# Kernel optimization log

Measured on AMD Instinct MI355X. Metric: run time of the kernel, lower is better.

## Reference

```python
import jax, jax.numpy as jnp
import numpy as np

DIM = 1024
NUM_HEADS = 16
NUM_KV_HEADS = 4
HEAD_DIM = DIM // NUM_HEADS
KV_DIM = NUM_KV_HEADS * HEAD_DIM
PARTIAL_ROPE_DIM = 32
ROPE_BASE = 10000.0
LORA_RANK = 4
NUM_LORA_STEPS = 2
LORA_SCALE = 1.0
B, S = 2, 2048


def _rms_norm(x):
    eps = jnp.asarray(jnp.finfo(x.dtype).eps, x.dtype)
    return x * jax.lax.rsqrt(jnp.mean(x * x, axis=-1, keepdims=True) + eps)


def _rope_cos_sin(seq_len, dtype):
    half = PARTIAL_ROPE_DIM // 2
    inv_freq = 1.0 / (ROPE_BASE ** (jnp.arange(0, PARTIAL_ROPE_DIM, 2, dtype=jnp.float32) / PARTIAL_ROPE_DIM))
    t = jnp.arange(seq_len, dtype=jnp.float32)
    freqs = jnp.outer(t, inv_freq)  # [S, half]
    return jnp.cos(freqs).astype(dtype), jnp.sin(freqs).astype(dtype)


def _apply_rope_partial(x, cos, sin):
    # x: [B, H, S, D]; rotate first PARTIAL_ROPE_DIM dims, pass the rest.
    half = PARTIAL_ROPE_DIM // 2
    x1 = x[..., :half]
    x2 = x[..., half:PARTIAL_ROPE_DIM]
    xp = x[..., PARTIAL_ROPE_DIM:]
    c = cos[None, None, :, :]
    s = sin[None, None, :, :]
    return jnp.concatenate([x1 * c + x2 * s, -x1 * s + x2 * c, xp], axis=-1)


def setup_inputs() -> dict:
    key = jax.random.key(0)
    ks = jax.random.split(key, 12)
    std = 0.02
    return {
        "x": jax.random.normal(ks[0], (B, S, DIM), jnp.float32),
        "Wq": jax.random.normal(ks[1], (DIM, DIM), jnp.float32) * std,
        "Wk": jax.random.normal(ks[2], (KV_DIM, DIM), jnp.float32) * std,
        "Wv": jax.random.normal(ks[3], (KV_DIM, DIM), jnp.float32) * std,
        "Wproj": jax.random.normal(ks[4], (DIM, DIM), jnp.float32) * std,
        "q_gain": jnp.full((NUM_HEADS,), 1.0, jnp.float32),
        "lora_A_q": jax.random.normal(ks[5], (NUM_LORA_STEPS, LORA_RANK, DIM), jnp.float32) * std,
        "lora_B_q": jax.random.normal(ks[6], (NUM_LORA_STEPS, DIM, LORA_RANK), jnp.float32) * std,
        "lora_A_v": jax.random.normal(ks[7], (NUM_LORA_STEPS, LORA_RANK, DIM), jnp.float32) * std,
        "lora_B_v": jax.random.normal(ks[8], (NUM_LORA_STEPS, KV_DIM, LORA_RANK), jnp.float32) * std,
        "step_idx": 0,
    }


def reference(x, Wq, Wk, Wv, Wproj, q_gain, lora_A_q, lora_B_q, lora_A_v, lora_B_v, step_idx):
    bsz, seqlen, dim = x.shape
    q = x @ Wq.T
    v = x @ Wv.T
    if 0 <= step_idx < NUM_LORA_STEPS:
        q = q + LORA_SCALE * ((x @ lora_A_q[step_idx].T) @ lora_B_q[step_idx].T)
        v = v + LORA_SCALE * ((x @ lora_A_v[step_idx].T) @ lora_B_v[step_idx].T)
    k = x @ Wk.T

    q = q.reshape(bsz, seqlen, NUM_HEADS, HEAD_DIM).transpose(0, 2, 1, 3)      # [B,H,S,D]
    k = k.reshape(bsz, seqlen, NUM_KV_HEADS, HEAD_DIM).transpose(0, 2, 1, 3)   # [B,Hkv,S,D]
    v = v.reshape(bsz, seqlen, NUM_KV_HEADS, HEAD_DIM).transpose(0, 2, 1, 3)

    q = _rms_norm(q)
    k = _rms_norm(k)

    cos, sin = _rope_cos_sin(seqlen, q.dtype)
    q = _apply_rope_partial(q, cos, sin)
    k = _apply_rope_partial(k, cos, sin)

    q = q * q_gain.astype(q.dtype)[None, :, None, None]

    # GQA causal SDPA
    groups = NUM_HEADS // NUM_KV_HEADS
    qg = q.reshape(bsz, NUM_KV_HEADS, groups, seqlen, HEAD_DIM)
    scale = 1.0 / np.sqrt(HEAD_DIM)
    scores = jnp.einsum('bkgsd,bktd->bkgst', qg, k) * scale  # [B,Hkv,G,S,S]
    causal = jnp.tril(jnp.ones((seqlen, seqlen), bool))
    scores = jnp.where(causal[None, None, None], scores, jnp.asarray(-jnp.inf, scores.dtype))
    attn = jax.nn.softmax(scores, axis=-1)
    y = jnp.einsum('bkgst,bktd->bkgsd', attn, v)
    y = y.reshape(bsz, NUM_HEADS, seqlen, HEAD_DIM).transpose(0, 2, 1, 3).reshape(bsz, seqlen, dim)
    return y @ Wproj.T
```

## Files before the change

kernel.cpp:

```cpp
#include <hip/hip_runtime.h>
#include <hip/hip_bf16.h>
#include <stdint.h>

#define DIM 1024
#define NH 16
#define NKV 4
#define HD 64
#define SEQ 2048
#define BATCH 2
#define RANK 4
#define NSTEPS 2

#define XN      4194304
#define WQ_END  5242880
#define WK_END  5505024
#define WV_END  5767168
#define CVT_BLOCKS 6656
#define LORA_BLOCKS 1024

typedef unsigned short u16;
typedef unsigned int u32;
typedef __attribute__((ext_vector_type(8))) __bf16 bf16x8;
typedef __attribute__((ext_vector_type(4))) float f32x4;

__device__ __forceinline__ float bf2f(u16 v) {
    u32 u = ((u32)v) << 16;
    return __builtin_bit_cast(float, u);
}
__device__ __forceinline__ u16 f2bf(float f) {
    u32 u = __builtin_bit_cast(u32, f);
    u32 r = (u + 0x7fffu + ((u >> 16) & 1u)) >> 16;
    return (u16)r;
}
__device__ __forceinline__ u32 pk2(float a, float b) {
    return (u32)f2bf(a) | ((u32)f2bf(b) << 16);
}
__device__ __forceinline__ u32 pk2t(float a, float b) {
    return __builtin_amdgcn_perm(__builtin_bit_cast(u32, b),
                                 __builtin_bit_cast(u32, a), 0x07060302u);
}
__device__ __forceinline__ void glds16(const u16* g, u16* l) {
    __builtin_amdgcn_global_load_lds(
        (const __attribute__((address_space(1))) u32*)g,
        (__attribute__((address_space(3))) u32*)l, 16, 0, 0);
}

__global__ __launch_bounds__(256) void k_prep(
    const float* __restrict__ x, const float* __restrict__ Wq,
    const float* __restrict__ Wk, const float* __restrict__ Wv,
    const float* __restrict__ Wp, u16* __restrict__ dst,
    const float* __restrict__ Aq, const float* __restrict__ Av,
    const int* __restrict__ step_p, float* __restrict__ tq, float* __restrict__ tv)
{
    int bx = blockIdx.x;
    if (bx < CVT_BLOCKS) {
        int e = (bx * 256 + threadIdx.x) * 4;
        const float* src;
        if (e < XN)          src = x  + e;
        else if (e < WQ_END) src = Wq + (e - XN);
        else if (e < WK_END) src = Wk + (e - WQ_END);
        else if (e < WV_END) src = Wv + (e - WK_END);
        else                 src = Wp + (e - WV_END);
        float4 v = *(const float4*)src;
        *(uint2*)(dst + e) = make_uint2(pk2(v.x, v.y), pk2(v.z, v.w));
        return;
    }
    int wave = ((bx - CVT_BLOCKS) * 256 + threadIdx.x) >> 6;
    int lane = threadIdx.x & 63;
    int step = step_p[0];
    int valid = (step >= 0 && step < NSTEPS);
    int sc = valid ? step : 0;
    const float* xr = x + wave * DIM + lane * 16;
    float xf[16];
#pragma unroll
    for (int q = 0; q < 4; q++) {
        float4 v4 = *(const float4*)(xr + q * 4);
        xf[q * 4 + 0] = v4.x; xf[q * 4 + 1] = v4.y;
        xf[q * 4 + 2] = v4.z; xf[q * 4 + 3] = v4.w;
    }
    float sums[8];
#pragma unroll
    for (int j = 0; j < 8; j++) {
        const float* ar = (j < 4 ? Aq + sc * RANK * DIM + j * DIM
                                 : Av + sc * RANK * DIM + (j - 4) * DIM) + lane * 16;
        float s = 0.f;
#pragma unroll
        for (int q = 0; q < 4; q++) {
            float4 a4 = *(const float4*)(ar + q * 4);
            s += xf[q * 4 + 0] * a4.x + xf[q * 4 + 1] * a4.y
               + xf[q * 4 + 2] * a4.z + xf[q * 4 + 3] * a4.w;
        }
#pragma unroll
        for (int o = 32; o > 0; o >>= 1) s += __shfl_xor(s, o, 64);
        sums[j] = s;
    }
    if (!valid) {
#pragma unroll
        for (int j = 0; j < 8; j++) sums[j] = 0.f;
    }
    if (lane == 0) {
        tq[wave * 4 + 0] = sums[0]; tq[wave * 4 + 1] = sums[1];
        tq[wave * 4 + 2] = sums[2]; tq[wave * 4 + 3] = sums[3];
        tv[wave * 4 + 0] = sums[4]; tv[wave * 4 + 1] = sums[5];
        tv[wave * 4 + 2] = sums[6]; tv[wave * 4 + 3] = sums[7];
    }
}

__global__ __launch_bounds__(256) void k_gemm_qkv(
    const u16* __restrict__ A, const u16* __restrict__ B,
    u16* __restrict__ qkv, u16* __restrict__ vtb,
    const float* __restrict__ tq, const float* __restrict__ Bq,
    const float* __restrict__ tv, const float* __restrict__ Bv,
    const float* __restrict__ gain, const int* __restrict__ step_p)
{
    __shared__ __align__(16) u16 As[16384];
    __shared__ __align__(16) u16 Bs[16384];
    int bx = blockIdx.x;
    int xcd = bx & 7, o = bx >> 3;
    int bm = xcd * 4 + (o & 3);
    int bn = o >> 2;
    int t = threadIdx.x, lane = t & 63, w = t >> 6;
    int wy = w >> 1, wx = w & 1;
    int wb = t & ~63;
    int quad = lane >> 4, n16 = lane & 15;
    f32x4 acc[4][4];
#pragma unroll
    for (int i = 0; i < 4; i++)
#pragma unroll
        for (int j = 0; j < 4; j++) acc[i][j] = (f32x4){0.f, 0.f, 0.f, 0.f};

    int goff[4];
#pragma unroll
    for (int u = 0; u < 4; u++) {
        int idx = u * 256 + t;
        int grp = idx >> 6;
        int q_ = (idx >> 4) & 3, m = idx & 15;
        goff[u] = ((grp >> 1) * 16 + m) * DIM + (grp & 1) * 32 + q_ * 8;
    }
    const u16* Ab = A + bm * 128 * DIM;
    const u16* Bb = B + bn * 128 * DIM;

#pragma unroll 1
    for (int kb = 0; kb < 8; kb++) {
        int k0 = kb * 128;
        __syncthreads();
#pragma unroll
        for (int u = 0; u < 4; u++)
            glds16(Ab + goff[u] + k0, As + (u * 256 + wb) * 8);
#pragma unroll
        for (int u = 0; u < 4; u++)
            glds16(Ab + goff[u] + k0 + 64, As + 8192 + (u * 256 + wb) * 8);
#pragma unroll
        for (int u = 0; u < 4; u++)
            glds16(Bb + goff[u] + k0, Bs + (u * 256 + wb) * 8);
#pragma unroll
        for (int u = 0; u < 4; u++)
            glds16(Bb + goff[u] + k0 + 64, Bs + 8192 + (u * 256 + wb) * 8);
        __syncthreads();
#pragma unroll
        for (int c = 0; c < 4; c++) {
            int sl = (c >> 1) * 8192, ch = c & 1;
            bf16x8 af[4], bfr[4];
#pragma unroll
            for (int i = 0; i < 4; i++)
                af[i] = *(const bf16x8*)(As + sl + (((wy * 4 + i) * 2 + ch) * 64 + lane) * 8);
#pragma unroll
            for (int j = 0; j < 4; j++)
                bfr[j] = *(const bf16x8*)(Bs + sl + (((wx * 4 + j) * 2 + ch) * 64 + lane) * 8);
#pragma unroll
            for (int i = 0; i < 4; i++)
#pragma unroll
                for (int j = 0; j < 4; j++)
                    acc[i][j] = __builtin_amdgcn_mfma_f32_16x16x32_bf16(af[i], bfr[j], acc[i][j], 0, 0, 0);
        }
    }

    int step = step_p[0];
    int sc = (step >= 0 && step < NSTEPS) ? step : 0;
    int row_base = bm * 128 + wy * 64 + quad * 4;

    if (bn < 10) {
        bool isq = (bn < 8);
        int h2 = isq ? (bn * 2 + wx) : ((bn - 8) * 2 + wx);
        int colbase = isq ? (h2 * 64) : (1024 + h2 * 64);
        if (isq) {
            float4 B4[4];
#pragma unroll
            for (int j = 0; j < 4; j++)
                B4[j] = *(const float4*)(Bq + (sc * DIM + h2 * 64 + j * 16 + n16) * RANK);
#pragma unroll
            for (int i = 0; i < 4; i++)
#pragma unroll
                for (int r = 0; r < 4; r++) {
                    float4 t4 = *(const float4*)(tq + (row_base + i * 16 + r) * 4);
#pragma unroll
                    for (int j = 0; j < 4; j++)
                        acc[i][j][r] += t4.x * B4[j].x + t4.y * B4[j].y
                                      + t4.z * B4[j].z + t4.w * B4[j].w;
                }
        }
        float postmul = isq ? (gain[h2] * 0.125f * 1.4426950408889634f) : 1.f;
        float invf = exp2f(-(float)n16 * 0.8304820237218405f);
#pragma unroll
        for (int i = 0; i < 4; i++)
#pragma unroll
            for (int r = 0; r < 4; r++) {
                float s = acc[i][0][r] * acc[i][0][r] + acc[i][1][r] * acc[i][1][r]
                        + acc[i][2][r] * acc[i][2][r] + acc[i][3][r] * acc[i][3][r];
#pragma unroll
                for (int o2 = 1; o2 < 16; o2 <<= 1) s += __shfl_xor(s, o2, 64);
                float rr = rsqrtf(s * (1.f / 64.f) + 1.1920928955078125e-7f);
                int row = row_base + i * 16 + r;
                float v0 = acc[i][0][r] * rr, v1 = acc[i][1][r] * rr;
                float v2 = acc[i][2][r] * rr, v3 = acc[i][3][r] * rr;
                float ang = (float)(row & 2047) * invf;
                float cs = cosf(ang), sn = sinf(ang);
                float o0 = v0 * cs + v1 * sn;
                float o1 = -v0 * sn + v1 * cs;
                u16* dst = qkv + row * 1536 + colbase + n16;
                dst[0]  = f2bf(o0 * postmul);
                dst[16] = f2bf(o1 * postmul);
                dst[32] = f2bf(v2 * postmul);
                dst[48] = f2bf(v3 * postmul);
            }
    } else {
        int g = (bn - 10) * 2 + wx;
        float4 B4[4];
#pragma unroll
        for (int j = 0; j < 4; j++)
            B4[j] = *(const float4*)(Bv + (sc * (NKV * HD) + g * 64 + j * 16 + n16) * RANK);
#pragma unroll
        for (int i = 0; i < 4; i++) {
#pragma unroll
            for (int r = 0; r < 4; r++) {
                float4 t4 = *(const float4*)(tv + (row_base + i * 16 + r) * 4);
#pragma unroll
                for (int j = 0; j < 4; j++)
                    acc[i][j][r] += t4.x * B4[j].x + t4.y * B4[j].y
                                  + t4.z * B4[j].z + t4.w * B4[j].w;
            }
            int row0 = row_base + i * 16;
            int b = row0 >> 11, s0 = row0 & 2047;
#pragma unroll
            for (int j = 0; j < 4; j++) {
                int d = j * 16 + n16;
                uint2 pkv = make_uint2(pk2(acc[i][j][0], acc[i][j][1]),
                                       pk2(acc[i][j][2], acc[i][j][3]));
                *(uint2*)(vtb + ((b * NKV + g) * HD + d) * SEQ + s0) = pkv;
            }
        }
    }
}

__global__ __launch_bounds__(256) void k_gemm_proj(
    const u16* __restrict__ A, const u16* __restrict__ B,
    float* __restrict__ C)
{
    __shared__ __align__(16) u16 As[16384];
    __shared__ __align__(16) u16 Bs[8192];
    int bx = blockIdx.x;
    int bn = (bx & 7) * 2 + ((bx >> 3) & 1);
    int bm = bx >> 4;
    int t = threadIdx.x, lane = t & 63, w = t >> 6;
    int wy = w >> 1, wx = w & 1;
    int wb = t & ~63;
    f32x4 acc[4][2];
#pragma unroll
    for (int i = 0; i < 4; i++)
#pragma unroll
        for (int j = 0; j < 2; j++) acc[i][j] = (f32x4){0.f, 0.f, 0.f, 0.f};

    int goffA[4], goffB[2];
#pragma unroll
    for (int u = 0; u < 4; u++) {
        int idx = u * 256 + t;
        int grp = idx >> 6;
        int q_ = (idx >> 4) & 3, m = idx & 15;
        goffA[u] = ((grp >> 1) * 16 + m) * DIM + (grp & 1) * 32 + q_ * 8;
    }
#pragma unroll
    for (int u = 0; u < 2; u++) {
        int idx = u * 256 + t;
        int grp = idx >> 6;
        int q_ = (idx >> 4) & 3, m = idx & 15;
        goffB[u] = ((grp >> 1) * 16 + m) * DIM + (grp & 1) * 32 + q_ * 8;
    }
    const u16* Ab = A + bm * 128 * DIM;
    const u16* Bb = B + bn * 64 * DIM;

#pragma unroll 1
    for (int kb = 0; kb < 8; kb++) {
        int k0 = kb * 128;
        __syncthreads();
#pragma unroll
        for (int u = 0; u < 4; u++)
            glds16(Ab + goffA[u] + k0, As + (u * 256 + wb) * 8);
#pragma unroll
        for (int u = 0; u < 4; u++)
            glds16(Ab + goffA[u] + k0 + 64, As + 8192 + (u * 256 + wb) * 8);
#pragma unroll
        for (int u = 0; u < 2; u++)
            glds16(Bb + goffB[u] + k0, Bs + (u * 256 + wb) * 8);
#pragma unroll
        for (int u = 0; u < 2; u++)
            glds16(Bb + goffB[u] + k0 + 64, Bs + 4096 + (u * 256 + wb) * 8);
        __syncthreads();
#pragma unroll
        for (int c = 0; c < 4; c++) {
            int slA = (c >> 1) * 8192, slB = (c >> 1) * 4096, ch = c & 1;
            bf16x8 af[4], bfr[2];
#pragma unroll
            for (int i = 0; i < 4; i++)
                af[i] = *(const bf16x8*)(As + slA + (((wy * 4 + i) * 2 + ch) * 64 + lane) * 8);
#pragma unroll
            for (int j = 0; j < 2; j++)
                bfr[j] = *(const bf16x8*)(Bs + slB + (((wx * 2 + j) * 2 + ch) * 64 + lane) * 8);
#pragma unroll
            for (int i = 0; i < 4; i++)
#pragma unroll
                for (int j = 0; j < 2; j++)
                    acc[i][j] = __builtin_amdgcn_mfma_f32_16x16x32_bf16(af[i], bfr[j], acc[i][j], 0, 0, 0);
        }
    }
    int quad = lane >> 4, n16 = lane & 15;
#pragma unroll
    for (int i = 0; i < 4; i++)
#pragma unroll
        for (int j = 0; j < 2; j++) {
            int col = bn * 64 + wx * 32 + j * 16 + n16;
#pragma unroll
            for (int r = 0; r < 4; r++) {
                int rowm = bm * 128 + wy * 64 + i * 16 + quad * 4 + r;
                C[rowm * DIM + col] = acc[i][j][r];
            }
        }
}

__global__ __launch_bounds__(256) void k_attn(
    const u16* __restrict__ qkv, const u16* __restrict__ vt,
    const float* __restrict__ gain, u16* __restrict__ y,
    float* __restrict__ accP, float* __restrict__ psP)
{
    __shared__ __align__(16) u16 kf[2][4096];
    __shared__ __align__(16) u16 vf[2][4096];
    __shared__ __align__(16) u16 pb[4][1024];
    int bx = blockIdx.x;
    int bgid = bx & 7, inner = bx >> 3;
    int b = bgid >> 2, g = bgid & 3;
    int h = g * 4 + (inner & 3);
    int qtsel = (inner >> 2) & 15;
    int role = (inner >> 6) & 1;
    int pairsel = (b * 16 + h) * 16 + qtsel;
    int t = threadIdx.x, lane = t & 63, w = t >> 6, wb = t & ~63;
    int quad = lane >> 4, n16 = lane & 15;
    float negM = -11.67f * fabsf(gain[h]);

    const u16* kbase = qkv + b * SEQ * 1536 + 1024 + g * HD;
    const u16* vbase = vt + (b * NKV + g) * HD * SEQ;

    int koff0, koff1, voff0, voff1;
    {
        int s0 = t, r0 = s0 >> 3, c0 = (s0 & 7) ^ (r0 & 7);
        koff0 = r0 * 1536 + c0 * 8;  voff0 = r0 * 2048 + c0 * 8;
        int s1 = 256 + t, r1 = s1 >> 3, c1 = (s1 & 7) ^ (r1 & 7);
        koff1 = r1 * 1536 + c1 * 8;  voff1 = r1 * 2048 + c1 * 8;
    }
    int swb = n16 & 7;
    int o0 = n16 * 8 + (quad ^ swb);
    int o1 = n16 * 8 + ((4 + quad) ^ swb);
    u16* pw = pb[w];

    f32x4 acc[4];
    float ps;
    bf16x8 qlo, qhi;
    int qrow;

    auto reset_acc = [&]() {
#pragma unroll
        for (int i = 0; i < 4; i++) acc[i] = (f32x4){0.f, 0.f, 0.f, 0.f};
        ps = 0.f;
    };
    auto load_q = [&](int qt) {
        qrow = qt * 64 + w * 16 + n16;
        const u16* qp = qkv + (b * SEQ + qrow) * 1536 + h * HD + quad * 8;
        qlo = *(const bf16x8*)qp;
        qhi = *(const bf16x8*)(qp + 32);
    };
    auto stage = [&](int kt, int p) {
        const u16* kp = kbase + kt * (64 * 1536);
        const u16* vp = vbase + kt * 64;
        glds16(kp + koff0, kf[p] + wb * 8);
        glds16(kp + koff1, kf[p] + (256 + wb) * 8);
        glds16(vp + voff0, vf[p] + wb * 8);
        glds16(vp + voff1, vf[p] + (256 + wb) * 8);
    };
    auto compute = [&](int kt, int p, bool diag) {
        f32x4 st[4];
#pragma unroll
        for (int nt = 0; nt < 4; nt++) {
            f32x4 sa = (f32x4){0.f, 0.f, 0.f, 0.f};
            sa = __builtin_amdgcn_mfma_f32_16x16x32_bf16(*(bf16x8*)(kf[p] + (nt * 128 + o0) * 8), qlo, sa, 0, 0, 0);
            sa = __builtin_amdgcn_mfma_f32_16x16x32_bf16(*(bf16x8*)(kf[p] + (nt * 128 + o1) * 8), qhi, sa, 0, 0, 0);
            st[nt] = sa;
        }
        float pr[4][4];
        if (diag) {
            int kb0 = kt * 64;
#pragma unroll
            for (int nt = 0; nt < 4; nt++)
#pragma unroll
                for (int r = 0; r < 4; r++) {
                    int key = kb0 + nt * 16 + quad * 4 + r;
                    float e = exp2f(st[nt][r] + negM);
                    e = (key > qrow) ? 0.f : e;
                    pr[nt][r] = e;
                    ps += e;
                }
        } else {
#pragma unroll
            for (int nt = 0; nt < 4; nt++)
#pragma unroll
                for (int r = 0; r < 4; r++) {
                    float e = exp2f(st[nt][r] + negM);
                    pr[nt][r] = e;
                    ps += e;
                }
        }
#pragma unroll
        for (int nt = 0; nt < 4; nt++) {
            u32 lo = pk2t(pr[nt][0], pr[nt][1]);
            u32 hi = pk2t(pr[nt][2], pr[nt][3]);
            int ck = nt >> 1;
            int qbk = (nt & 1) * 2 + (quad >> 1);
            int byteoff = (ck * 64 + qbk * 16 + n16) * 16 + (quad & 1) * 8;
            *(uint2*)((char*)pw + byteoff) = make_uint2(lo, hi);
        }
        asm volatile("s_waitcnt lgkmcnt(0)" ::: "memory");
#pragma unroll
        for (int ck = 0; ck < 2; ck++) {
            bf16x8 pfr = *(bf16x8*)(pw + (ck * 64 + lane) * 8);
            int oo = ck ? o1 : o0;
#pragma unroll
            for (int dt = 0; dt < 4; dt++)
                acc[dt] = __builtin_amdgcn_mfma_f32_16x16x32_bf16(*(bf16x8*)(vf[p] + (dt * 128 + oo) * 8), pfr, acc[dt], 0, 0, 0);
        }
        asm volatile("" ::: "memory");
    };
    auto run = [&](int kt0, int kt1, bool diag_last) {
        int p = 0;
        stage(kt0, 0);
#pragma unroll 1
        for (int kt = kt0; kt < kt1; kt++) {
            if (kt + 1 < kt1) {
                stage(kt + 1, p ^ 1);
                asm volatile("s_waitcnt vmcnt(4)" ::: "memory");
            } else {
                asm volatile("s_waitcnt vmcnt(0)" ::: "memory");
            }
            __builtin_amdgcn_s_barrier();
            compute(kt, p, diag_last && (kt == kt1 - 1));
            asm volatile("s_waitcnt lgkmcnt(0)" ::: "memory");
            __builtin_amdgcn_s_barrier();
            p ^= 1;
        }
    };
    auto write_partial = [&](int pidx) {
        float pt = ps + __shfl_xor(ps, 16, 64);
        pt += __shfl_xor(pt, 32, 64);
        if (quad == 0) psP[pidx * 64 + w * 16 + n16] = pt;
        float* ap = accP + pidx * 4096 + w * 1024;
#pragma unroll
        for (int dt = 0; dt < 4; dt++)
#pragma unroll
            for (int r = 0; r < 4; r++)
                ap[dt * 256 + quad * 64 + r * 16 + n16] = acc[dt][r];
    };

    if (role == 0) {
        load_q(qtsel);
        reset_acc();
        run(0, qtsel + 1, true);
        {
            float pt = ps + __shfl_xor(ps, 16, 64);
            pt += __shfl_xor(pt, 32, 64);
            float li = 1.f / pt;
#pragma unroll
            for (int dt = 0; dt < 4; dt++) {
                uint2 o = make_uint2(pk2(acc[dt][0] * li, acc[dt][1] * li),
                                     pk2(acc[dt][2] * li, acc[dt][3] * li));
                int d = dt * 16 + quad * 4;
                *(uint2*)(y + (b * SEQ + qrow) * DIM + h * HD + d) = o;
            }
        }
        load_q(31 - qtsel);
        reset_acc();
        run(0, 16 - qtsel, false);
        write_partial(pairsel * 2);
    } else {
        load_q(31 - qtsel);
        reset_acc();
        run(16 - qtsel, 32 - qtsel, true);
        write_partial(pairsel * 2 + 1);
    }
}

__global__ __launch_bounds__(256) void k_comb(
    const float* __restrict__ accP, const float* __restrict__ psP,
    u16* __restrict__ y)
{
    int pairsel = blockIdx.x;
    int b = pairsel >> 8, h = (pairsel >> 4) & 15, qtsel = pairsel & 15;
    int qt = 31 - qtsel;
    int t = threadIdx.x, w = t >> 6, d = t & 63;
    const float* a0 = accP + (pairsel * 2) * 4096 + t * 16;
    const float* a1 = a0 + 4096;
    const float* p0 = psP + pairsel * 128 + w * 16;
    const float* p1 = p0 + 64;
    u16* yp = y + (b * SEQ + qt * 64 + w * 16) * DIM + h * HD + d;
#pragma unroll
    for (int i = 0; i < 4; i++) {
        float4 v0 = *(const float4*)(a0 + i * 4);
        float4 v1 = *(const float4*)(a1 + i * 4);
        float4 s0 = *(const float4*)(p0 + i * 4);
        float4 s1 = *(const float4*)(p1 + i * 4);
        yp[(i * 4 + 0) * DIM] = f2bf((v0.x + v1.x) / (s0.x + s1.x));
        yp[(i * 4 + 1) * DIM] = f2bf((v0.y + v1.y) / (s0.y + s1.y));
        yp[(i * 4 + 2) * DIM] = f2bf((v0.z + v1.z) / (s0.z + s1.z));
        yp[(i * 4 + 3) * DIM] = f2bf((v0.w + v1.w) / (s0.w + s1.w));
    }
}

extern "C" void kernel_launch(void* const* d_in, const int* in_sizes, int n_in,
                              void* d_out, int out_size, void* d_ws, size_t ws_size,
                              hipStream_t stream)
{
    (void)in_sizes; (void)n_in; (void)out_size; (void)ws_size;
    const float* x     = (const float*)d_in[0];
    const float* Wq    = (const float*)d_in[1];
    const float* Wk    = (const float*)d_in[2];
    const float* Wv    = (const float*)d_in[3];
    const float* Wproj = (const float*)d_in[4];
    const float* qgain = (const float*)d_in[5];
    const float* Aq    = (const float*)d_in[6];
    const float* Bq    = (const float*)d_in[7];
    const float* Av    = (const float*)d_in[8];
    const float* Bv    = (const float*)d_in[9];
    const int*   step  = (const int*)d_in[10];

    char* ws = (char*)d_ws;
    u16* wsbf = (u16*)ws;
    u16* xb   = wsbf;
    u16* wf   = wsbf + XN;
    u16* wp   = wsbf + WV_END;
    u16* qkv  = (u16*)(ws + 13631488);
    float* tq = (float*)(ws + 26214400);
    float* tv = tq + 16384;
    float* psP = (float*)(ws + 26345472);
    u16* vt   = (u16*)(ws + 26607616);
    float* accP = (float*)d_out;
    u16* y    = xb;

    k_prep<<<CVT_BLOCKS + LORA_BLOCKS, 256, 0, stream>>>(x, Wq, Wk, Wv, Wproj, wsbf,
                                                         Aq, Av, step, tq, tv);
    k_gemm_qkv<<<384, 256, 0, stream>>>(xb, wf, qkv, vt, tq, Bq, tv, Bv, qgain, step);
    k_attn<<<1024, 256, 0, stream>>>(qkv, vt, qgain, y, accP, psP);
    k_comb<<<512, 256, 0, stream>>>(accP, psP, y);
    k_gemm_proj<<<512, 256, 0, stream>>>(y, wp, (float*)d_out);
}
```

Before: 230.6 us.

## Drop attention split-K combine kernel and halve GEMM K-tile

Attention blocks no longer split the long causal q-tile across two roles with fp32 partials. Each block now processes its short and long q-tile fully and writes normalized bf16 output directly, which removes the k_comb kernel and the partial-buffer traffic. Both GEMMs use a 64-wide K step with half the shared memory, trading more barriers for lower LDS footprint. The attention grid halves to 512 blocks, reducing parallelism and lengthening per-block work.

```diff
diff --git a/kernel.cpp b/kernel.cpp
--- a/kernel.cpp
+++ b/kernel.cpp
@@ -113,8 +113,8 @@
     const float* __restrict__ tv, const float* __restrict__ Bv,
     const float* __restrict__ gain, const int* __restrict__ step_p)
 {
-    __shared__ __align__(16) u16 As[16384];
-    __shared__ __align__(16) u16 Bs[16384];
+    __shared__ __align__(16) u16 As[8192];
+    __shared__ __align__(16) u16 Bs[8192];
     int bx = blockIdx.x;
     int xcd = bx & 7, o = bx >> 3;
     int bm = xcd * 4 + (o & 3);
@@ -141,32 +141,25 @@
     const u16* Bb = B + bn * 128 * DIM;
 
 #pragma unroll 1
-    for (int kb = 0; kb < 8; kb++) {
-        int k0 = kb * 128;
+    for (int kb = 0; kb < 16; kb++) {
+        int k0 = kb * 64;
         __syncthreads();
 #pragma unroll
         for (int u = 0; u < 4; u++)
             glds16(Ab + goff[u] + k0, As + (u * 256 + wb) * 8);
 #pragma unroll
         for (int u = 0; u < 4; u++)
-            glds16(Ab + goff[u] + k0 + 64, As + 8192 + (u * 256 + wb) * 8);
-#pragma unroll
-        for (int u = 0; u < 4; u++)
             glds16(Bb + goff[u] + k0, Bs + (u * 256 + wb) * 8);
-#pragma unroll
-        for (int u = 0; u < 4; u++)
-            glds16(Bb + goff[u] + k0 + 64, Bs + 8192 + (u * 256 + wb) * 8);
         __syncthreads();
 #pragma unroll
-        for (int c = 0; c < 4; c++) {
-            int sl = (c >> 1) * 8192, ch = c & 1;
+        for (int c = 0; c < 2; c++) {
             bf16x8 af[4], bfr[4];
 #pragma unroll
             for (int i = 0; i < 4; i++)
-                af[i] = *(const bf16x8*)(As + sl + (((wy * 4 + i) * 2 + ch) * 64 + lane) * 8);
+                af[i] = *(const bf16x8*)(As + (((wy * 4 + i) * 2 + c) * 64 + lane) * 8);
 #pragma unroll
             for (int j = 0; j < 4; j++)
-                bfr[j] = *(const bf16x8*)(Bs + sl + (((wx * 4 + j) * 2 + ch) * 64 + lane) * 8);
+                bfr[j] = *(const bf16x8*)(Bs + (((wx * 4 + j) * 2 + c) * 64 + lane) * 8);
 #pragma unroll
             for (int i = 0; i < 4; i++)
 #pragma unroll
@@ -256,8 +249,8 @@
     const u16* __restrict__ A, const u16* __restrict__ B,
     float* __restrict__ C)
 {
-    __shared__ __align__(16) u16 As[16384];
-    __shared__ __align__(16) u16 Bs[8192];
+    __shared__ __align__(16) u16 As[8192];
+    __shared__ __align__(16) u16 Bs[4096];
     int bx = blockIdx.x;
     int bn = (bx & 7) * 2 + ((bx >> 3) & 1);
     int bm = bx >> 4;
@@ -289,32 +282,25 @@
     const u16* Bb = B + bn * 64 * DIM;
 
 #pragma unroll 1
-    for (int kb = 0; kb < 8; kb++) {
-        int k0 = kb * 128;
+    for (int kb = 0; kb < 16; kb++) {
+        int k0 = kb * 64;
         __syncthreads();
 #pragma unroll
         for (int u = 0; u < 4; u++)
             glds16(Ab + goffA[u] + k0, As + (u * 256 + wb) * 8);
 #pragma unroll
-        for (int u = 0; u < 4; u++)
-            glds16(Ab + goffA[u] + k0 + 64, As + 8192 + (u * 256 + wb) * 8);
-#pragma unroll
         for (int u = 0; u < 2; u++)
             glds16(Bb + goffB[u] + k0, Bs + (u * 256 + wb) * 8);
-#pragma unroll
-        for (int u = 0; u < 2; u++)
-            glds16(Bb + goffB[u] + k0 + 64, Bs + 4096 + (u * 256 + wb) * 8);
         __syncthreads();
 #pragma unroll
-        for (int c = 0; c < 4; c++) {
-            int slA = (c >> 1) * 8192, slB = (c >> 1) * 4096, ch = c & 1;
+        for (int c = 0; c < 2; c++) {
             bf16x8 af[4], bfr[2];
 #pragma unroll
             for (int i = 0; i < 4; i++)
-                af[i] = *(const bf16x8*)(As + slA + (((wy * 4 + i) * 2 + ch) * 64 + lane) * 8);
+                af[i] = *(const bf16x8*)(As + (((wy * 4 + i) * 2 + c) * 64 + lane) * 8);
 #pragma unroll
             for (int j = 0; j < 2; j++)
-                bfr[j] = *(const bf16x8*)(Bs + slB + (((wx * 2 + j) * 2 + ch) * 64 + lane) * 8);
+                bfr[j] = *(const bf16x8*)(Bs + (((wx * 2 + j) * 2 + c) * 64 + lane) * 8);
 #pragma unroll
             for (int i = 0; i < 4; i++)
 #pragma unroll
@@ -338,8 +324,7 @@
 
 __global__ __launch_bounds__(256) void k_attn(
     const u16* __restrict__ qkv, const u16* __restrict__ vt,
-    const float* __restrict__ gain, u16* __restrict__ y,
-    float* __restrict__ accP, float* __restrict__ psP)
+    const float* __restrict__ gain, u16* __restrict__ y)
 {
     __shared__ __align__(16) u16 kf[2][4096];
     __shared__ __align__(16) u16 vf[2][4096];
@@ -349,8 +334,6 @@
     int b = bgid >> 2, g = bgid & 3;
     int h = g * 4 + (inner & 3);
     int qtsel = (inner >> 2) & 15;
-    int role = (inner >> 6) & 1;
-    int pairsel = (b * 16 + h) * 16 + qtsel;
     int t = threadIdx.x, lane = t & 63, w = t >> 6, wb = t & ~63;
     int quad = lane >> 4, n16 = lane & 15;
     float negM = -11.67f * fabsf(gain[h]);
@@ -464,70 +447,27 @@
             p ^= 1;
         }
     };
-    auto write_partial = [&](int pidx) {
+    auto finish = [&]() {
         float pt = ps + __shfl_xor(ps, 16, 64);
         pt += __shfl_xor(pt, 32, 64);
-        if (quad == 0) psP[pidx * 64 + w * 16 + n16] = pt;
-        float* ap = accP + pidx * 4096 + w * 1024;
-#pragma unroll
-        for (int dt = 0; dt < 4; dt++)
-#pragma unroll
-            for (int r = 0; r < 4; r++)
-                ap[dt * 256 + quad * 64 + r * 16 + n16] = acc[dt][r];
+        float li = 1.f / pt;
+#pragma unroll
+        for (int dt = 0; dt < 4; dt++) {
+            uint2 o = make_uint2(pk2(acc[dt][0] * li, acc[dt][1] * li),
+                                 pk2(acc[dt][2] * li, acc[dt][3] * li));
+            int d = dt * 16 + quad * 4;
+            *(uint2*)(y + (b * SEQ + qrow) * DIM + h * HD + d) = o;
+        }
     };
 
-    if (role == 0) {
-        load_q(qtsel);
-        reset_acc();
-        run(0, qtsel + 1, true);
-        {
-            float pt = ps + __shfl_xor(ps, 16, 64);
-            pt += __shfl_xor(pt, 32, 64);
-            float li = 1.f / pt;
-#pragma unroll
-            for (int dt = 0; dt < 4; dt++) {
-                uint2 o = make_uint2(pk2(acc[dt][0] * li, acc[dt][1] * li),
-                                     pk2(acc[dt][2] * li, acc[dt][3] * li));
-                int d = dt * 16 + quad * 4;
-                *(uint2*)(y + (b * SEQ + qrow) * DIM + h * HD + d) = o;
-            }
-        }
-        load_q(31 - qtsel);
-        reset_acc();
-        run(0, 16 - qtsel, false);
-        write_partial(pairsel * 2);
-    } else {
-        load_q(31 - qtsel);
-        reset_acc();
-        run(16 - qtsel, 32 - qtsel, true);
-        write_partial(pairsel * 2 + 1);
-    }
-}
-
-__global__ __launch_bounds__(256) void k_comb(
-    const float* __restrict__ accP, const float* __restrict__ psP,
-    u16* __restrict__ y)
-{
-    int pairsel = blockIdx.x;
-    int b = pairsel >> 8, h = (pairsel >> 4) & 15, qtsel = pairsel & 15;
-    int qt = 31 - qtsel;
-    int t = threadIdx.x, w = t >> 6, d = t & 63;
-    const float* a0 = accP + (pairsel * 2) * 4096 + t * 16;
-    const float* a1 = a0 + 4096;
-    const float* p0 = psP + pairsel * 128 + w * 16;
-    const float* p1 = p0 + 64;
-    u16* yp = y + (b * SEQ + qt * 64 + w * 16) * DIM + h * HD + d;
-#pragma unroll
-    for (int i = 0; i < 4; i++) {
-        float4 v0 = *(const float4*)(a0 + i * 4);
-        float4 v1 = *(const float4*)(a1 + i * 4);
-        float4 s0 = *(const float4*)(p0 + i * 4);
-        float4 s1 = *(const float4*)(p1 + i * 4);
-        yp[(i * 4 + 0) * DIM] = f2bf((v0.x + v1.x) / (s0.x + s1.x));
-        yp[(i * 4 + 1) * DIM] = f2bf((v0.y + v1.y) / (s0.y + s1.y));
-        yp[(i * 4 + 2) * DIM] = f2bf((v0.z + v1.z) / (s0.z + s1.z));
-        yp[(i * 4 + 3) * DIM] = f2bf((v0.w + v1.w) / (s0.w + s1.w));
-    }
+    load_q(qtsel);
+    reset_acc();
+    run(0, qtsel + 1, true);
+    finish();
+    load_q(31 - qtsel);
+    reset_acc();
+    run(0, 32 - qtsel, true);
+    finish();
 }
 
 extern "C" void kernel_launch(void* const* d_in, const int* in_sizes, int n_in,
@@ -555,15 +495,12 @@
     u16* qkv  = (u16*)(ws + 13631488);
     float* tq = (float*)(ws + 26214400);
     float* tv = tq + 16384;
-    float* psP = (float*)(ws + 26345472);
     u16* vt   = (u16*)(ws + 26607616);
-    float* accP = (float*)d_out;
     u16* y    = xb;
 
     k_prep<<<CVT_BLOCKS + LORA_BLOCKS, 256, 0, stream>>>(x, Wq, Wk, Wv, Wproj, wsbf,
                                                          Aq, Av, step, tq, tv);
     k_gemm_qkv<<<384, 256, 0, stream>>>(xb, wf, qkv, vt, tq, Bq, tv, Bv, qgain, step);
-    k_attn<<<1024, 256, 0, stream>>>(qkv, vt, qgain, y, accP, psP);
-    k_comb<<<512, 256, 0, stream>>>(accP, psP, y);
+    k_attn<<<512, 256, 0, stream>>>(qkv, vt, qgain, y);
     k_gemm_proj<<<512, 256, 0, stream>>>(y, wp, (float*)d_out);
 }
```

After: 209.1 us. 9.3% less time.
